# Kernel tuning notes

Hardware: AMD Instinct MI355X
Metric: run time of the kernel (lower is better)

Reference implementation:

```python
import jax, jax.numpy as jnp
import numpy as np

LN_EPS = 1e-12


def setup_inputs() -> dict:
    key = jax.random.key(0)
    ks = jax.random.split(key, 5)
    B, N, D_IN, D_OUT, E = 32, 2048, 128, 128, 64
    return {
        "x": jax.random.normal(ks[0], (B, N, D_IN), dtype=jnp.float32),
        "node_embeddings": jax.random.normal(ks[1], (N, E), dtype=jnp.float32),
        "time_embeddings": jax.random.normal(ks[2], (E,), dtype=jnp.float32),
        "weights_pool": jax.random.normal(ks[3], (E, 2, D_IN, D_OUT), dtype=jnp.float32) * 0.02,
        "bias_pool": jax.random.normal(ks[4], (E, D_OUT), dtype=jnp.float32) * 0.02,
        "ln_weight": jnp.ones((E,), dtype=jnp.float32),
        "ln_bias": jnp.zeros((E,), dtype=jnp.float32),
    }


def reference(x, node_embeddings, time_embeddings, weights_pool, bias_pool, ln_weight, ln_bias):
    # e: [N, E] = LayerNorm(node_emb + time_emb)  (dropout in eval mode = identity)
    e = node_embeddings + time_embeddings[None, :]
    mu = jnp.mean(e, axis=-1, keepdims=True)
    var = jnp.mean(jnp.square(e - mu), axis=-1, keepdims=True)
    e = (e - mu) * jax.lax.rsqrt(var + LN_EPS) * ln_weight + ln_bias

    # adaptive adjacency: softmax over rows of e @ e.T  -> [N, N]
    adj = jax.nn.softmax(jnp.einsum('nd,md->nm', e, e), axis=1)

    # per-node weights [N, 2, I, O] and bias [N, O]
    weights = jnp.einsum('nd,dkio->nkio', e, weights_pool)
    bias = e @ bias_pool  # [N, O]

    # supports: k=0 identity (x itself), k=1 adjacency aggregation
    x_agg = jnp.einsum('nm,bmc->bnc', adj, x)        # [B, N, I]
    x_g = jnp.stack([x, x_agg], axis=2)              # [B, N, 2, I]

    # per-node batched GEMM + bias
    out = jnp.einsum('bnki,nkio->bno', x_g, weights) + bias
    return out
```

## Files before the change

### kernel.cpp

```cpp
#include <hip/hip_runtime.h>


typedef unsigned short u16;
typedef unsigned int u32;
typedef __attribute__((ext_vector_type(8))) short bf16x8;
typedef __attribute__((ext_vector_type(4))) short bf16x4;
typedef __attribute__((ext_vector_type(4))) float f32x4;
typedef const __attribute__((address_space(1))) u16* gas1;
typedef __attribute__((address_space(3))) u16* las3;

#define NN 2048
#define EE 64
#define CC 128
#define BB 32

__device__ __forceinline__ u16 f2bf(float f) {
  u32 u = __builtin_bit_cast(u32, f);
  u += 0x7fffu + ((u >> 16) & 1u);
  return (u16)(u >> 16);
}

__device__ __forceinline__ f32x4 mfma16(bf16x8 a, bf16x8 b, f32x4 c) {
  return __builtin_amdgcn_mfma_f32_16x16x32_bf16(a, b, c, 0, 0, 0);
}

__global__ __launch_bounds__(256) void k_mega0(
    const float* __restrict__ x, const float* __restrict__ ne,
    const float* __restrict__ te, const float* __restrict__ pool,
    const float* __restrict__ bias_pool, const float* __restrict__ lnw,
    const float* __restrict__ lnb,
    float* __restrict__ e, u16* __restrict__ e_bf, float* __restrict__ bias_out,
    u16* __restrict__ pool_r, u16* __restrict__ x_t, u16* __restrict__ xg_t) {
  __shared__ __align__(16) char smem[33280];
  int bid = blockIdx.x;
  int tid = threadIdx.x;
  if (bid < 512) {
    float* sh = (float*)smem;
    int nw = tid >> 6, d = tid & 63;
    int n = bid * 4 + nw;
    float v = ne[n * EE + d] + te[d];
    float s = v;
#pragma unroll
    for (int off = 32; off > 0; off >>= 1) s += __shfl_xor(s, off);
    float mean = s * (1.0f / 64.0f);
    float c = v - mean;
    float q = c * c;
#pragma unroll
    for (int off = 32; off > 0; off >>= 1) q += __shfl_xor(q, off);
    float inv = rsqrtf(q * (1.0f / 64.0f) + 1e-12f);
    float ev = c * inv * lnw[d] + lnb[d];
    e[n * EE + d] = ev;
    e_bf[n * EE + d] = f2bf(ev);
    sh[nw * 64 + d] = ev;
    __syncthreads();
#pragma unroll
    for (int oo = 0; oo < 2; ++oo) {
      int o = oo * 64 + d;
      float acc = 0.f;
#pragma unroll 8
      for (int dd = 0; dd < 64; ++dd) acc += sh[nw * 64 + dd] * bias_pool[dd * CC + o];
      bias_out[n * CC + o] = acc;
    }
  } else if (bid < 768) {
    float* t = (float*)smem;
    int ki = bid - 512;
    for (int it = 0; it < 32; ++it) {
      int idx = it * 256 + tid;
      int d = idx >> 7, o = idx & 127;
      t[o * 65 + d] = pool[d * 32768 + ki * 128 + o];
    }
    __syncthreads();
    for (int it = 0; it < 32; ++it) {
      int idx = it * 256 + tid;
      int o = idx >> 6, d = idx & 63;
      pool_r[((size_t)o * 256 + ki) * 64 + d] = f2bf(t[o * 65 + d]);
    }
  } else {
    u16* t = (u16*)smem;
    int bx = bid - 768;
    int b = bx >> 5;
    int m0 = (bx & 31) * 64;
    for (int it = 0; it < 32; ++it) {
      int idx = it * 256 + tid;
      int m = idx >> 7, c = idx & 127;
      float v = x[((size_t)b * NN + m0 + m) * CC + c];
      t[c * 68 + m] = f2bf(v);
    }
    __syncthreads();
    for (int it = 0; it < 32; ++it) {
      int idx = it * 256 + tid;
      int c = idx >> 6, m = idx & 63;
      x_t[((size_t)b * CC + c) * NN + m0 + m] = t[c * 68 + m];
    }
    for (int it = 0; it < 16; ++it) {
      int idx = it * 256 + tid;
      int m = idx >> 6, c2 = idx & 63;
      float2 v = *(const float2*)&x[((size_t)b * NN + m0 + m) * CC + c2 * 2];
      u32 pk = (u32)f2bf(v.x) | ((u32)f2bf(v.y) << 16);
      *(u32*)&xg_t[(((size_t)(m0 + m)) * 32 + b) * 256 + c2 * 2] = pk;
    }
  }
}

__global__ __launch_bounds__(256) void k_Sexp(const float* __restrict__ e,
                                              u16* __restrict__ P,
                                              float* __restrict__ rs) {
  __shared__ float er[64 * 68];
  __shared__ float ec[64 * 68];
  int n0 = (blockIdx.x >> 5) * 64, m0 = (blockIdx.x & 31) * 64;
  int tid = threadIdx.x;
  for (int it = 0; it < 16; ++it) {
    int idx = it * 256 + tid;
    int r = idx >> 6, d = idx & 63;
    er[r * 68 + d] = e[(n0 + r) * EE + d];
    ec[r * 68 + d] = e[(m0 + r) * EE + d];
  }
  __syncthreads();
  int tx = tid & 15, ty = tid >> 4;
  float acc[4][4] = {};
  for (int d4 = 0; d4 < 64; d4 += 4) {
    f32x4 av[4], bv[4];
#pragma unroll
    for (int i = 0; i < 4; ++i) av[i] = *(const f32x4*)&er[(ty + 16 * i) * 68 + d4];
#pragma unroll
    for (int j = 0; j < 4; ++j) bv[j] = *(const f32x4*)&ec[(tx + 16 * j) * 68 + d4];
#pragma unroll
    for (int i = 0; i < 4; ++i)
#pragma unroll
      for (int j = 0; j < 4; ++j) {
        acc[i][j] += av[i][0] * bv[j][0];
        acc[i][j] += av[i][1] * bv[j][1];
        acc[i][j] += av[i][2] * bv[j][2];
        acc[i][j] += av[i][3] * bv[j][3];
      }
  }
#pragma unroll
  for (int i = 0; i < 4; ++i) {
    float s = 0.f;
#pragma unroll
    for (int j = 0; j < 4; ++j) {
      float pv = __expf(acc[i][j]);
      P[(size_t)(n0 + ty + 16 * i) * NN + m0 + tx + 16 * j] = f2bf(pv);
      s += pv;
    }
#pragma unroll
    for (int off = 8; off > 0; off >>= 1) s += __shfl_xor(s, off);
    if (tx == 0) atomicAdd(&rs[n0 + ty + 16 * i], s);
  }
}

__global__ __launch_bounds__(256, 4) void k_aggr(
    const u16* __restrict__ P, const u16* __restrict__ x_t,
    const float* __restrict__ rs, u16* __restrict__ xg_t) {
  __shared__ __align__(16) char smem[32768];
  int tid = threadIdx.x;
  int lane = tid & 63, w = tid >> 6;
  int lm = lane & 15, lq = lane >> 4;
  u16* As = (u16*)smem;
  u16* Bs = (u16*)(smem + 16384);
  int b = blockIdx.x & 31, mb = blockIdx.x >> 5;
  int n0 = mb * 128;
  int wm = w >> 1, wn = w & 1;
  f32x4 acc[4][4] = {};
  const u16* a_src = P + (size_t)n0 * NN;
  const u16* b_src = x_t + (size_t)b * CC * NN;
  for (int kc = 0; kc < NN; kc += 64) {
    __syncthreads();
#pragma unroll
    for (int ii = 0; ii < 4; ++ii) {
      int idx = ii * 256 + tid;
      int row = idx >> 3, ch = idx & 7;
      int sc = kc + ((ch ^ (row & 7)) << 3);
      __builtin_amdgcn_global_load_lds((gas1)(a_src + (size_t)row * NN + sc),
                                       (las3)(As + (size_t)(ii * 256 + w * 64) * 8), 16, 0, 0);
      __builtin_amdgcn_global_load_lds((gas1)(b_src + (size_t)row * NN + sc),
                                       (las3)(Bs + (size_t)(ii * 256 + w * 64) * 8), 16, 0, 0);
    }
    __syncthreads();
#pragma unroll
    for (int kk = 0; kk < 64; kk += 32) {
      int cb = (kk >> 3) + lq;
      bf16x8 af[4], bq[4];
#pragma unroll
      for (int i = 0; i < 4; ++i) {
        int row = wm * 64 + i * 16 + lm;
        af[i] = *(const bf16x8*)&As[row * 64 + ((cb ^ (row & 7)) << 3)];
      }
#pragma unroll
      for (int j = 0; j < 4; ++j) {
        int row = wn * 64 + j * 16 + lm;
        bq[j] = *(const bf16x8*)&Bs[row * 64 + ((cb ^ (row & 7)) << 3)];
      }
#pragma unroll
      for (int i = 0; i < 4; ++i)
#pragma unroll
        for (int j = 0; j < 4; ++j)
          acc[i][j] = mfma16(af[i], bq[j], acc[i][j]);
    }
  }
#pragma unroll
  for (int i = 0; i < 4; ++i) {
    int nr = n0 + wm * 64 + i * 16 + lq * 4;
#pragma unroll
    for (int r = 0; r < 4; ++r) {
      float sc = 1.0f / rs[nr + r];
#pragma unroll
      for (int j = 0; j < 4; ++j) {
        int c = wn * 64 + j * 16 + lm;
        xg_t[((size_t)(nr + r) * 32 + b) * 256 + 128 + c] = f2bf(acc[i][j][r] * sc);
      }
    }
  }
}

#define GA_OS 36
#define GA_NS 584
__global__ __launch_bounds__(256, 4) void k_genapply(
    const u16* __restrict__ e_bf, const u16* __restrict__ pool_r,
    const u16* __restrict__ xg_t, const float* __restrict__ biasb,
    float* __restrict__ out) {
  __shared__ u16 W[2][16 * GA_NS];
  int tid = threadIdx.x;
  int lane = tid & 63, w = tid >> 6;
  int lm = lane & 15, lq = lane >> 4;
  int x = blockIdx.x & 7, k = blockIdx.x >> 3;
  int og = k & 7, ng = x * 16 + (k >> 3);
  int n0 = ng * 16, o0 = og * 16;

  bf16x8 eB[2];
#pragma unroll
  for (int ks = 0; ks < 2; ++ks)
    eB[ks] = *(const bf16x8*)&e_bf[(n0 + lm) * EE + ks * 32 + lq * 8];

  auto GEN = [&](int kt) {
    u16* Wb = &W[kt & 1][0];
    int ki0 = kt * 32;
#pragma unroll
    for (int ot = 0; ot < 4; ++ot) {
      int o_l = w * 4 + ot;
      const u16* pb = pool_r + ((size_t)(o0 + o_l) * 256 + ki0 + lm) * 64 + lq * 8;
#pragma unroll
      for (int kc = 0; kc < 2; ++kc) {
        const u16* ap = pb + kc * 16 * 64;
        bf16x8 a0 = *(const bf16x8*)ap;
        bf16x8 a1 = *(const bf16x8*)(ap + 32);
        f32x4 d = {0.f, 0.f, 0.f, 0.f};
        d = mfma16(a0, eB[0], d);
        d = mfma16(a1, eB[1], d);
        ushort4 h;
        h.x = f2bf(d[0]); h.y = f2bf(d[1]); h.z = f2bf(d[2]); h.w = f2bf(d[3]);
        *(ushort4*)&Wb[lm * GA_NS + o_l * GA_OS + kc * 16 + lq * 4] = h;
      }
    }
  };

  f32x4 acc[4][2] = {};
  GEN(0);
  __syncthreads();

  for (int kt = 0; kt < 8; ++kt) {
    int ki0 = kt * 32;
    const u16* Wb = &W[kt & 1][0];
    bf16x8 xv[4][2];
    bf16x4 wlo[4], whi[4];
#pragma unroll
    for (int i = 0; i < 4; ++i) {
      int n_l = w * 4 + i;
      const u16* xp = xg_t + ((size_t)(n0 + n_l) * 32) * 256 + ki0 + lq * 8;
      xv[i][0] = *(const bf16x8*)(xp + lm * 256);
      xv[i][1] = *(const bf16x8*)(xp + (16 + lm) * 256);
      const u16* wp = &Wb[n_l * GA_NS + lm * GA_OS + lq * 8];
      wlo[i] = *(const bf16x4*)wp;
      whi[i] = *(const bf16x4*)(wp + 4);
    }
    if (kt < 7) GEN(kt + 1);
#pragma unroll
    for (int i = 0; i < 4; ++i) {
      bf16x8 wA = __builtin_shufflevector(wlo[i], whi[i], 0, 1, 2, 3, 4, 5, 6, 7);
      acc[i][0] = mfma16(wA, xv[i][0], acc[i][0]);
      acc[i][1] = mfma16(wA, xv[i][1], acc[i][1]);
    }
    __syncthreads();
  }

#pragma unroll
  for (int i = 0; i < 4; ++i) {
    int n = n0 + w * 4 + i;
    float4 bv = *(const float4*)&biasb[n * CC + o0 + lq * 4];
#pragma unroll
    for (int bt = 0; bt < 2; ++bt) {
      int b = bt * 16 + lm;
      float4 o4;
      o4.x = acc[i][bt][0] + bv.x;
      o4.y = acc[i][bt][1] + bv.y;
      o4.z = acc[i][bt][2] + bv.z;
      o4.w = acc[i][bt][3] + bv.w;
      *(float4*)&out[((size_t)b * NN + n) * CC + o0 + lq * 4] = o4;
    }
  }
}

extern "C" void kernel_launch(void* const* d_in, const int* in_sizes, int n_in,
                              void* d_out, int out_size, void* d_ws, size_t ws_size,
                              hipStream_t stream) {
  const float* x        = (const float*)d_in[0];
  const float* node_emb = (const float*)d_in[1];
  const float* time_emb = (const float*)d_in[2];
  const float* pool     = (const float*)d_in[3];
  const float* bias_pl  = (const float*)d_in[4];
  const float* ln_w     = (const float*)d_in[5];
  const float* ln_b     = (const float*)d_in[6];
  float* out = (float*)d_out;

  char* p = (char*)d_ws;
  auto alloc = [&](size_t bytes) {
    char* r = p;
    p += (bytes + 255) & ~(size_t)255;
    return r;
  };
  float* e      = (float*)alloc((size_t)NN * EE * 4);
  u16*   e_bf   = (u16*)  alloc((size_t)NN * EE * 2);
  float* biasb  = (float*)alloc((size_t)NN * CC * 4);
  u16*   Pm     = (u16*)  alloc((size_t)NN * NN * 2);
  float* rs     = (float*)alloc((size_t)NN * 4);
  u16*   x_t    = (u16*)  alloc((size_t)BB * CC * NN * 2);
  u16*   xg_t   = (u16*)  alloc((size_t)NN * BB * 256 * 2);
  u16*   pool_r = (u16*)  alloc((size_t)128 * 256 * 64 * 2);

  if (ws_size < (size_t)(p - (char*)d_ws)) return;

  (void)hipMemsetAsync(rs, 0, (size_t)NN * 4, stream);

  k_mega0<<<1792, 256, 0, stream>>>(x, node_emb, time_emb, pool, bias_pl, ln_w, ln_b,
                                    e, e_bf, biasb, pool_r, x_t, xg_t);
  k_Sexp<<<1024, 256, 0, stream>>>(e, Pm, rs);
  k_aggr<<<512, 256, 0, stream>>>(Pm, x_t, rs, xg_t);
  k_genapply<<<1024, 256, 0, stream>>>(e_bf, pool_r, xg_t, biasb, out);
}
```

Measured before the change: 259.4 us.

## Restructure genapply to 128-thread blocks with per-wave batch split and unrolled pipeline

k_genapply now runs with 128 threads per block instead of 256. Each of its two waves generates 8 output columns of the per-node weight tile and accumulates all 16 nodes for its own 16 batch rows. The k-loop is fully unrolled, and the GEN-next/APPLY-current interleave is kept. Plain __syncthreads is replaced by an LDS-only waitcnt plus s_barrier, so global loads are not drained at each barrier. The intent is better global load scheduling and a lighter barrier. In exchange, each wave does twice the weight generation, and the launch bound changes occupancy and register pressure.

```diff
diff --git a/kernel.cpp b/kernel.cpp
--- a/kernel.cpp
+++ b/kernel.cpp
@@ -215,7 +215,7 @@
 
 #define GA_OS 36
 #define GA_NS 584
-__global__ __launch_bounds__(256, 4) void k_genapply(
+__global__ __launch_bounds__(128, 2) void k_genapply(
     const u16* __restrict__ e_bf, const u16* __restrict__ pool_r,
     const u16* __restrict__ xg_t, const float* __restrict__ biasb,
     float* __restrict__ out) {
@@ -232,12 +232,11 @@
   for (int ks = 0; ks < 2; ++ks)
     eB[ks] = *(const bf16x8*)&e_bf[(n0 + lm) * EE + ks * 32 + lq * 8];
 
-  auto GEN = [&](int kt) {
-    u16* Wb = &W[kt & 1][0];
+  auto GEN = [&](int kt, u16* Wb) {
     int ki0 = kt * 32;
 #pragma unroll
-    for (int ot = 0; ot < 4; ++ot) {
-      int o_l = w * 4 + ot;
+    for (int ot = 0; ot < 8; ++ot) {
+      int o_l = w * 8 + ot;
       const u16* pb = pool_r + ((size_t)(o0 + o_l) * 256 + ki0 + lm) * 64 + lq * 8;
 #pragma unroll
       for (int kc = 0; kc < 2; ++kc) {
@@ -254,49 +253,44 @@
     }
   };
 
-  f32x4 acc[4][2] = {};
-  GEN(0);
-  __syncthreads();
-
+  f32x4 acc[16] = {};
+  const u16* xbase = xg_t + (size_t)n0 * 32 * 256 + (w * 16 + lm) * 256 + lq * 8;
+
+  auto APPLY = [&](int kt, const u16* Wb) {
+    int ki0 = kt * 32;
+#pragma unroll
+    for (int i = 0; i < 16; ++i) {
+      const u16* wp = &Wb[i * GA_NS + lm * GA_OS + lq * 8];
+      bf16x4 wlo = *(const bf16x4*)wp;
+      bf16x4 whi = *(const bf16x4*)(wp + 4);
+      bf16x8 wA = __builtin_shufflevector(wlo, whi, 0, 1, 2, 3, 4, 5, 6, 7);
+      bf16x8 xv = *(const bf16x8*)(xbase + (size_t)i * 32 * 256 + ki0);
+      acc[i] = mfma16(wA, xv, acc[i]);
+    }
+  };
+
+  GEN(0, &W[0][0]);
+  asm volatile("s_waitcnt lgkmcnt(0)" ::: "memory");
+  __builtin_amdgcn_s_barrier();
+#pragma unroll
   for (int kt = 0; kt < 8; ++kt) {
-    int ki0 = kt * 32;
-    const u16* Wb = &W[kt & 1][0];
-    bf16x8 xv[4][2];
-    bf16x4 wlo[4], whi[4];
-#pragma unroll
-    for (int i = 0; i < 4; ++i) {
-      int n_l = w * 4 + i;
-      const u16* xp = xg_t + ((size_t)(n0 + n_l) * 32) * 256 + ki0 + lq * 8;
-      xv[i][0] = *(const bf16x8*)(xp + lm * 256);
-      xv[i][1] = *(const bf16x8*)(xp + (16 + lm) * 256);
-      const u16* wp = &Wb[n_l * GA_NS + lm * GA_OS + lq * 8];
-      wlo[i] = *(const bf16x4*)wp;
-      whi[i] = *(const bf16x4*)(wp + 4);
-    }
-    if (kt < 7) GEN(kt + 1);
-#pragma unroll
-    for (int i = 0; i < 4; ++i) {
-      bf16x8 wA = __builtin_shufflevector(wlo[i], whi[i], 0, 1, 2, 3, 4, 5, 6, 7);
-      acc[i][0] = mfma16(wA, xv[i][0], acc[i][0]);
-      acc[i][1] = mfma16(wA, xv[i][1], acc[i][1]);
-    }
-    __syncthreads();
-  }
-
-#pragma unroll
-  for (int i = 0; i < 4; ++i) {
-    int n = n0 + w * 4 + i;
+    if (kt < 7) GEN(kt + 1, &W[(kt + 1) & 1][0]);
+    APPLY(kt, &W[kt & 1][0]);
+    asm volatile("s_waitcnt lgkmcnt(0)" ::: "memory");
+    __builtin_amdgcn_s_barrier();
+  }
+
+  int b = w * 16 + lm;
+#pragma unroll
+  for (int i = 0; i < 16; ++i) {
+    int n = n0 + i;
     float4 bv = *(const float4*)&biasb[n * CC + o0 + lq * 4];
-#pragma unroll
-    for (int bt = 0; bt < 2; ++bt) {
-      int b = bt * 16 + lm;
-      float4 o4;
-      o4.x = acc[i][bt][0] + bv.x;
-      o4.y = acc[i][bt][1] + bv.y;
-      o4.z = acc[i][bt][2] + bv.z;
-      o4.w = acc[i][bt][3] + bv.w;
-      *(float4*)&out[((size_t)b * NN + n) * CC + o0 + lq * 4] = o4;
-    }
+    float4 o4;
+    o4.x = acc[i][0] + bv.x;
+    o4.y = acc[i][1] + bv.y;
+    o4.z = acc[i][2] + bv.z;
+    o4.w = acc[i][3] + bv.w;
+    *(float4*)&out[((size_t)b * NN + n) * CC + o0 + lq * 4] = o4;
   }
 }
 
@@ -335,5 +329,5 @@
                                     e, e_bf, biasb, pool_r, x_t, xg_t);
   k_Sexp<<<1024, 256, 0, stream>>>(e, Pm, rs);
   k_aggr<<<512, 256, 0, stream>>>(Pm, x_t, rs, xg_t);
-  k_genapply<<<1024, 256, 0, stream>>>(e_bf, pool_r, xg_t, biasb, out);
-}
+  k_genapply<<<1024, 128, 0, stream>>>(e_bf, pool_r, xg_t, biasb, out);
+}
```

New measurement: 259.6 us. About the same (+0.1%).
